# Kernel tuning notes

Measured on AMD Instinct MI355X. Metric: run time of the kernel, lower is better.

The kernel has to match this reference:

```python
import math
import jax, jax.numpy as jnp
import numpy as np

H = 8
DIM = 256
HD = DIM // H
SCALE = math.sqrt(HD)
EPS = 1e-16


def _segment_softmax(scores, dst, num_nodes):
    # scores: [E, H], dst: [E] -> softmax over edges sharing the same dst
    m = jax.ops.segment_max(scores, dst, num_segments=num_nodes)  # [N, H]
    m = jnp.where(jnp.isfinite(m), m, 0.0)  # empty segments -> -inf -> 0
    e = jnp.exp(scores - m[dst])
    s = jax.ops.segment_sum(e, dst, num_segments=num_nodes)  # [N, H]
    return e / (s[dst] + EPS)


def _graph_attention(x, edges, wq, bq, wk, bk, wv, bv, wo, bo):
    # x: [N, DIM]; edges: [2, E] (src, dst). Dropout is identity (eval mode).
    N = x.shape[0]
    Q = (x @ wq + bq).reshape(N, H, HD)
    K = (x @ wk + bk).reshape(N, H, HD)
    V = (x @ wv + bv).reshape(N, H, HD)
    src, dst = edges[0], edges[1]
    scores = jnp.einsum('ehd,ehd->eh', Q[dst], K[src]) / SCALE  # [E, H]
    attn = _segment_softmax(scores, dst, N)  # [E, H]
    msgs = V[src] * attn[:, :, None]  # [E, H, HD]
    out = jax.ops.segment_sum(msgs, dst, num_segments=N).reshape(N, DIM)
    return out @ wo + bo


def _linear_params(key, fan_in, fan_out):
    k1, k2 = jax.random.split(key)
    bound = 1.0 / math.sqrt(fan_in)
    w = jax.random.uniform(k1, (fan_in, fan_out), minval=-bound, maxval=bound, dtype=jnp.float32)
    b = jax.random.uniform(k2, (fan_out,), minval=-bound, maxval=bound, dtype=jnp.float32)
    return w, b


def setup_inputs() -> dict:
    key = jax.random.key(0)
    ks = jax.random.split(key, 12)
    n_slot, n_dom = 20000, 1000
    e_slot, e_dom = 320000, 16000
    inp = {
        'slot_x': jax.random.normal(ks[0], (n_slot, DIM), dtype=jnp.float32),
        'domain_x': jax.random.normal(ks[1], (n_dom, DIM), dtype=jnp.float32),
        'slot_edges': jax.random.randint(ks[2], (2, e_slot), 0, n_slot, dtype=jnp.int32),
        'domain_edges': jax.random.randint(ks[3], (2, e_dom), 0, n_dom, dtype=jnp.int32),
    }
    names = ['wq', 'wk', 'wv', 'wo']
    for i, nm in enumerate(names):
        w, b = _linear_params(ks[4 + i], DIM, DIM)
        inp[f'slot_{nm}'] = w
        inp[f'slot_{nm}_b'] = b
    for i, nm in enumerate(names):
        w, b = _linear_params(ks[8 + i], DIM, DIM)
        inp[f'dom_{nm}'] = w
        inp[f'dom_{nm}_b'] = b
    return inp


def reference(slot_x, domain_x, slot_edges, domain_edges,
              slot_wq, slot_wq_b, slot_wk, slot_wk_b, slot_wv, slot_wv_b, slot_wo, slot_wo_b,
              dom_wq, dom_wq_b, dom_wk, dom_wk_b, dom_wv, dom_wv_b, dom_wo, dom_wo_b):
    # slot branch: self-attention on slot graph + identity residual
    slot_out = _graph_attention(slot_x, slot_edges,
                                slot_wq, slot_wq_b, slot_wk, slot_wk_b,
                                slot_wv, slot_wv_b, slot_wo, slot_wo_b) + slot_x
    # domain branch
    dom_out = _graph_attention(domain_x, domain_edges,
                               dom_wq, dom_wq_b, dom_wk, dom_wk_b,
                               dom_wv, dom_wv_b, dom_wo, dom_wo_b) + domain_x
    return slot_out, dom_out
```

## Files before the change

### kernel.cpp

```cpp
#include <hip/hip_runtime.h>
#include <hip/hip_bf16.h>

#define DIM 256
#define INV_SCALE 0.17677669529663687f
#define SM_EPS 1e-16f
#define CAP 64
#define EPT 4

typedef unsigned short ushortT;
typedef unsigned int uintT;
typedef __attribute__((ext_vector_type(8))) __bf16 bf16x8;
typedef __attribute__((ext_vector_type(4))) float f32x4;

__device__ __forceinline__ float bf2f(ushortT u) {
    return __uint_as_float(((uintT)u) << 16);
}
__device__ __forceinline__ ushortT f2bf(float f) {
    uintT u = __float_as_uint(f);
    u += 0x7FFFu + ((u >> 16) & 1u);
    return (ushortT)(u >> 16);
}
template <int CTRL>
__device__ __forceinline__ float qperm_add(float p) {
    int v = __builtin_amdgcn_update_dpp(0, __float_as_int(p), CTRL, 0xF, 0xF, true);
    return p + __int_as_float(v);
}

struct WPack { const void* w[8]; const void* b[8]; };

__device__ __forceinline__ bool sniff_m16(const ushortT* __restrict__ x) {
    int lane = threadIdx.x & 63;
    ushortT u = x[lane * 2];
    int e = (u >> 7) & 0xFF;
    bool sane = ((u & 0x7FFFu) == 0) || (e >= 0x66 && e <= 0x90);
    unsigned long long m = __ballot(sane);
    return __popcll(m) >= 32;
}

__global__ __launch_bounds__(256) void megaA(
        const void* __restrict__ xs, const void* __restrict__ xd,
        const ushortT* __restrict__ sniff_src,
        ushortT* __restrict__ xb_s, ushortT* __restrict__ xb_d,
        WPack pk, ushortT* __restrict__ wT, float* __restrict__ biasF,
        int* __restrict__ flagWs,
        const int* __restrict__ src_s, const int* __restrict__ dst_s,
        const int* __restrict__ src_d, const int* __restrict__ dst_d,
        int* __restrict__ cnt_s, int* __restrict__ cnt_d,
        int* __restrict__ col_s, int* __restrict__ col_d,
        int Es_, int Ed_, int nSc,
        int n4s, int n4d, int nA0, int nA1)
{
    const int bid = blockIdx.x;
    const int t = threadIdx.x;

    if (bid < nSc) {
        const int base = bid * (256 * EPT) + t;
        #pragma unroll
        for (int u = 0; u < EPT; ++u) {
            const int idx = base + u * 256;
            if (idx < Es_) {
                const int dv = dst_s[idx];
                const int pos = atomicAdd(&cnt_s[dv], 1);
                if (pos < CAP) col_s[(dv << 6) + pos] = src_s[idx];
            } else {
                const int e = idx - Es_;
                if (e < Ed_) {
                    const int dv = dst_d[e];
                    const int pos = atomicAdd(&cnt_d[dv], 1);
                    if (pos < CAP) col_d[(dv << 6) + pos] = src_d[e];
                }
            }
        }
        return;
    }
    const bool m16 = sniff_m16(sniff_src);
    const int li2 = bid - nSc;

    if (li2 < nA0 + nA1) {
        const bool d = li2 >= nA0;
        const int li = d ? li2 - nA0 : li2;
        const int n4 = d ? n4d : n4s;
        const int i = li * 256 + t;
        if (i >= n4) return;
        const void* x = d ? xd : xs;
        ushortT* xb = d ? xb_d : xb_s;
        if (m16) {
            ((ushort4*)xb)[i] = ((const ushort4*)x)[i];
        } else {
            float4 v = ((const float4*)x)[i];
            ushort4 o2;
            o2.x = f2bf(v.x); o2.y = f2bf(v.y); o2.z = f2bf(v.z); o2.w = f2bf(v.w);
            ((ushort4*)xb)[i] = o2;
        }
    } else if (li2 < nA0 + nA1 + 128) {
        __shared__ float sh[64][65];
        const int r0 = li2 - (nA0 + nA1);
        const int which = r0 >> 4;
        const int tile = r0 & 15;
        const int tr = tile >> 2, tc = tile & 3;
        const void* w = pk.w[which];
        const int tx = t & 63, tg = t >> 6;
        #pragma unroll
        for (int i = 0; i < 16; ++i) {
            const int r = i * 4 + tg;
            const size_t si = (size_t)(tr * 64 + r) * 256 + tc * 64 + tx;
            sh[r][tx] = m16 ? bf2f(((const ushortT*)w)[si]) : ((const float*)w)[si];
        }
        __syncthreads();
        ushortT* o = wT + (size_t)which * 65536;
        #pragma unroll
        for (int i = 0; i < 16; ++i) {
            const int r = i * 4 + tg;
            o[(size_t)(tc * 64 + r) * 256 + tr * 64 + tx] = f2bf(sh[tx][r]);
        }
    } else if (li2 < nA0 + nA1 + 136) {
        const int which = li2 - (nA0 + nA1 + 128);
        const void* b = pk.b[which];
        float v = m16 ? bf2f(((const ushortT*)b)[t]) : ((const float*)b)[t];
        biasF[which * 256 + t] = v;
    } else {
        if (t == 0) *flagWs = m16 ? 1 : 0;
    }
}

__global__ __launch_bounds__(256, 2) void megaB(
        const ushortT* __restrict__ xb_s, const ushortT* __restrict__ xb_d,
        const ushortT* __restrict__ wT, const float* __restrict__ biasF,
        ushortT* __restrict__ q_s, ushortT* __restrict__ kv_s,
        ushortT* __restrict__ q_d, ushortT* __restrict__ kv_d,
        int Ms, int Md, int nbs_, int nbq_)
{
    const int bid = blockIdx.x;
    const int by  = bid / nbq_;
    const int bx0 = bid % nbq_;
    const bool dom = bx0 >= nbs_;
    const int bx = dom ? bx0 - nbs_ : bx0;
    const ushortT* A = dom ? xb_d : xb_s;
    const int M = dom ? Md : Ms;
    const int wbase = dom ? 4 : 0;
    ushortT* Q = dom ? q_d : q_s;
    ushortT* KV = dom ? kv_d : kv_s;

    __shared__ ushortT As[64 * 256];

    const int tid  = threadIdx.x;
    const int wid  = tid >> 6;
    const int lane = tid & 63;
    const int m    = lane & 15;
    const int q    = lane >> 4;
    const int row0 = bx * 64;
    const int col0 = by * 64;
    const int colw = col0 + wid * 16 + m;

    {
        const int r  = tid >> 2;
        const int qt = tid & 3;
        const size_t rowAddr = (size_t)min(row0 + r, M - 1) * DIM;
        const int xr = r & 7;
        #pragma unroll
        for (int j = 0; j < 8; ++j) {
            const int chunk = qt * 8 + j;
            uint4 v = *(const uint4*)(A + rowAddr + chunk * 8);
            *(uint4*)&As[r * 256 + ((chunk ^ xr) * 8)] = v;
        }
    }

    const ushortT* Bp = wT + (size_t)wbase * 65536 + (size_t)colw * DIM + q * 8;
    bf16x8 bl[8][3];
    #pragma unroll
    for (int kk = 0; kk < 8; ++kk)
        #pragma unroll
        for (int z = 0; z < 3; ++z)
            bl[kk][z] = *(const bf16x8*)(Bp + (size_t)z * 65536 + kk * 32);

    f32x4 acc[3][4];
    #pragma unroll
    for (int z = 0; z < 3; ++z)
        #pragma unroll
        for (int i = 0; i < 4; ++i)
            acc[z][i] = (f32x4){0.f, 0.f, 0.f, 0.f};

    const int xm = m & 7;

    __syncthreads();

    #pragma unroll
    for (int kk = 0; kk < 8; ++kk) {
        bf16x8 af[4];
        #pragma unroll
        for (int i = 0; i < 4; ++i)
            af[i] = *(const bf16x8*)&As[(i * 16 + m) * 256 + (((q + 4 * kk) ^ xm) * 8)];
        #pragma unroll
        for (int z = 0; z < 3; ++z)
            #pragma unroll
            for (int i = 0; i < 4; ++i)
                acc[z][i] = __builtin_amdgcn_mfma_f32_16x16x32_bf16(bl[kk][z], af[i], acc[z][i], 0, 0, 0);
    }

    const int colbase = col0 + wid * 16 + q * 4;
    #pragma unroll
    for (int z = 0; z < 3; ++z) {
        const float4 b4 = *(const float4*)&biasF[(wbase + z) * 256 + colbase];
        #pragma unroll
        for (int i = 0; i < 4; ++i) {
            const int row = row0 + i * 16 + m;
            if (row < M) {
                ushort4 o;
                o.x = f2bf(acc[z][i][0] + b4.x);
                o.y = f2bf(acc[z][i][1] + b4.y);
                o.z = f2bf(acc[z][i][2] + b4.z);
                o.w = f2bf(acc[z][i][3] + b4.w);
                ushortT* C = (z == 0)
                    ? (Q + (size_t)row * DIM + colbase)
                    : (KV + (size_t)row * 512 + (z - 1) * 256 + colbase);
                *(ushort4*)C = o;
            }
        }
    }
}

__global__ __launch_bounds__(256) void attn_kernel(
        const ushortT* __restrict__ Qs, const ushortT* __restrict__ KVs,
        const int* __restrict__ cnts, const int* __restrict__ css,
        ushortT* __restrict__ aggs,
        const ushortT* __restrict__ Qd_, const ushortT* __restrict__ KVd_,
        const int* __restrict__ cntd, const int* __restrict__ csd,
        ushortT* __restrict__ aggd,
        int Ns_, int Ntot)
{
    const int g = blockIdx.x * 4 + (threadIdx.x >> 6);
    if (g >= Ntot) return;
    const bool dom = g >= Ns_;
    const int d = dom ? g - Ns_ : g;
    const int t = threadIdx.x & 63;
    const ushortT* Qb = dom ? Qd_ : Qs;
    const ushortT* KVb = dom ? KVd_ : KVs;
    const int* cnt = dom ? cntd : cnts;
    const int* colsrc = dom ? csd : css;
    ushortT* aggb = dom ? aggd : aggs;

    const uintT t4 = (uintT)t * 4;
    const size_t cbase = (size_t)d * DIM + t4;
    uint2 qv = *(const uint2*)(Qb + cbase);
    const float q0 = bf2f((ushortT)(qv.x & 0xFFFF)), q1 = bf2f((ushortT)(qv.x >> 16));
    const float q2 = bf2f((ushortT)(qv.y & 0xFFFF)), q3 = bf2f((ushortT)(qv.y >> 16));

    float a0 = 0.f, a1 = 0.f, a2 = 0.f, a3 = 0.f, den = 0.f;

    auto PROC = [&](uint2 kvc, uint2 vvc) {
        float k0 = bf2f((ushortT)(kvc.x & 0xFFFF)), k1 = bf2f((ushortT)(kvc.x >> 16));
        float k2 = bf2f((ushortT)(kvc.y & 0xFFFF)), k3 = bf2f((ushortT)(kvc.y >> 16));
        float p = q0 * k0 + q1 * k1 + q2 * k2 + q3 * k3;
        p = qperm_add<0xB1>(p);
        p = qperm_add<0x4E>(p);
        p += __shfl_xor(p, 4, 8);
        const float w = __expf(fminf(p * INV_SCALE, 60.0f));
        den += w;
        a0 += w * bf2f((ushortT)(vvc.x & 0xFFFF));
        a1 += w * bf2f((ushortT)(vvc.x >> 16));
        a2 += w * bf2f((ushortT)(vvc.y & 0xFFFF));
        a3 += w * bf2f((ushortT)(vvc.y >> 16));
    };

    int deg = cnt[d];
    if (deg > CAP) deg = CAP;
    const int* cl = colsrc + ((size_t)d << 6);
    int i = 0;
    for (; i + 8 <= deg; i += 8) {
        const int4 c0 = *(const int4*)(cl + i);
        const int4 c1 = *(const int4*)(cl + i + 4);
        const uintT o0 = ((uintT)c0.x << 9) + t4;
        const uintT o1 = ((uintT)c0.y << 9) + t4;
        const uintT o2 = ((uintT)c0.z << 9) + t4;
        const uintT o3 = ((uintT)c0.w << 9) + t4;
        const uintT o4 = ((uintT)c1.x << 9) + t4;
        const uintT o5 = ((uintT)c1.y << 9) + t4;
        const uintT o6 = ((uintT)c1.z << 9) + t4;
        const uintT o7 = ((uintT)c1.w << 9) + t4;
        uint2 k0v = *(const uint2*)(KVb + o0), v0v = *(const uint2*)(KVb + o0 + 256);
        uint2 k1v = *(const uint2*)(KVb + o1), v1v = *(const uint2*)(KVb + o1 + 256);
        uint2 k2v = *(const uint2*)(KVb + o2), v2v = *(const uint2*)(KVb + o2 + 256);
        uint2 k3v = *(const uint2*)(KVb + o3), v3v = *(const uint2*)(KVb + o3 + 256);
        uint2 k4v = *(const uint2*)(KVb + o4), v4v = *(const uint2*)(KVb + o4 + 256);
        uint2 k5v = *(const uint2*)(KVb + o5), v5v = *(const uint2*)(KVb + o5 + 256);
        uint2 k6v = *(const uint2*)(KVb + o6), v6v = *(const uint2*)(KVb + o6 + 256);
        uint2 k7v = *(const uint2*)(KVb + o7), v7v = *(const uint2*)(KVb + o7 + 256);
        PROC(k0v, v0v); PROC(k1v, v1v); PROC(k2v, v2v); PROC(k3v, v3v);
        PROC(k4v, v4v); PROC(k5v, v5v); PROC(k6v, v6v); PROC(k7v, v7v);
    }
    for (; i + 4 <= deg; i += 4) {
        const int4 c0 = *(const int4*)(cl + i);
        const uintT o0 = ((uintT)c0.x << 9) + t4;
        const uintT o1 = ((uintT)c0.y << 9) + t4;
        const uintT o2 = ((uintT)c0.z << 9) + t4;
        const uintT o3 = ((uintT)c0.w << 9) + t4;
        uint2 k0v = *(const uint2*)(KVb + o0), v0v = *(const uint2*)(KVb + o0 + 256);
        uint2 k1v = *(const uint2*)(KVb + o1), v1v = *(const uint2*)(KVb + o1 + 256);
        uint2 k2v = *(const uint2*)(KVb + o2), v2v = *(const uint2*)(KVb + o2 + 256);
        uint2 k3v = *(const uint2*)(KVb + o3), v3v = *(const uint2*)(KVb + o3 + 256);
        PROC(k0v, v0v); PROC(k1v, v1v); PROC(k2v, v2v); PROC(k3v, v3v);
    }
    for (; i < deg; ++i) {
        const uintT sb = ((uintT)cl[i] << 9) + t4;
        uint2 kv = *(const uint2*)(KVb + sb);
        uint2 vv = *(const uint2*)(KVb + sb + 256);
        PROC(kv, vv);
    }

    const float r = 1.0f / (den + SM_EPS);
    ushort4 o;
    o.x = f2bf(a0 * r); o.y = f2bf(a1 * r); o.z = f2bf(a2 * r); o.w = f2bf(a3 * r);
    *(ushort4*)(aggb + cbase) = o;
}

__global__ __launch_bounds__(256, 2) void gemm_out(
        const ushortT* __restrict__ As_, const ushortT* __restrict__ Ad_,
        const ushortT* __restrict__ wT, const float* __restrict__ biasF,
        const void* __restrict__ xs, const void* __restrict__ xd,
        void* __restrict__ dout, int Ms, int Md, int nbs,
        const int* __restrict__ flag)
{
    const bool dom = (int)blockIdx.x >= nbs;
    const int bx = dom ? blockIdx.x - nbs : blockIdx.x;
    const ushortT* A = dom ? Ad_ : As_;
    const int M = dom ? Md : Ms;
    const int widx = 3 + (dom ? 4 : 0);
    const ushortT* BT = wT + (size_t)widx * 65536;
    const float* bias = biasF + widx * 256;
    const void* res = dom ? xd : xs;
    const size_t outOff = dom ? (size_t)Ms * DIM : 0;

    __shared__ ushortT As2[64 * 256];

    const int tid  = threadIdx.x;
    const int wid  = tid >> 6;
    const int lane = tid & 63;
    const int m    = lane & 15;
    const int q    = lane >> 4;
    const int row0 = bx * 64;
    const int col0 = blockIdx.y * 64;
    const int colw = col0 + wid * 16 + m;

    {
        const int r  = tid >> 2;
        const int qt = tid & 3;
        const size_t rowAddr = (size_t)min(row0 + r, M - 1) * DIM;
        const int xr = r & 7;
        #pragma unroll
        for (int j = 0; j < 8; ++j) {
            const int chunk = qt * 8 + j;
            uint4 v = *(const uint4*)(A + rowAddr + chunk * 8);
            *(uint4*)&As2[r * 256 + ((chunk ^ xr) * 8)] = v;
        }
    }

    const ushortT* Bp = BT + (size_t)colw * DIM + q * 8;
    bf16x8 bl[8];
    #pragma unroll
    for (int kk = 0; kk < 8; ++kk)
        bl[kk] = *(const bf16x8*)(Bp + kk * 32);

    f32x4 acc[4];
    #pragma unroll
    for (int i = 0; i < 4; ++i) acc[i] = (f32x4){0.f, 0.f, 0.f, 0.f};

    const int xm = m & 7;

    __syncthreads();

    #pragma unroll
    for (int kk = 0; kk < 8; ++kk) {
        bf16x8 af[4];
        #pragma unroll
        for (int i = 0; i < 4; ++i)
            af[i] = *(const bf16x8*)&As2[(i * 16 + m) * 256 + (((q + 4 * kk) ^ xm) * 8)];
        #pragma unroll
        for (int i = 0; i < 4; ++i)
            acc[i] = __builtin_amdgcn_mfma_f32_16x16x32_bf16(bl[kk], af[i], acc[i], 0, 0, 0);
    }

    const bool m16 = (*flag != 0);
    const int colbase = col0 + wid * 16 + q * 4;
    const float4 b4 = *(const float4*)&bias[colbase];
    #pragma unroll
    for (int i = 0; i < 4; ++i) {
        const int row = row0 + i * 16 + m;
        if (row < M) {
            const size_t ridx = (size_t)row * DIM + colbase;
            float v0 = acc[i][0] + b4.x, v1 = acc[i][1] + b4.y;
            float v2 = acc[i][2] + b4.z, v3 = acc[i][3] + b4.w;
            if (m16) {
                ushort4 rv = *(const ushort4*)((const ushortT*)res + ridx);
                v0 += bf2f(rv.x); v1 += bf2f(rv.y); v2 += bf2f(rv.z); v3 += bf2f(rv.w);
                ushort4 o;
                o.x = f2bf(v0); o.y = f2bf(v1); o.z = f2bf(v2); o.w = f2bf(v3);
                *(ushort4*)((ushortT*)dout + outOff + ridx) = o;
            } else {
                float4 rv = *(const float4*)((const float*)res + ridx);
                float4 o;
                o.x = v0 + rv.x; o.y = v1 + rv.y; o.z = v2 + rv.z; o.w = v3 + rv.w;
                *(float4*)((float*)dout + outOff + ridx) = o;
            }
        }
    }
}

extern "C" void kernel_launch(void* const* d_in, const int* in_sizes, int n_in,
                              void* d_out, int out_size, void* d_ws, size_t ws_size,
                              hipStream_t stream)
{
    const void* slot_x = d_in[0];
    const void* dom_x  = d_in[1];
    const int* slot_edges = (const int*)d_in[2];
    const int* dom_edges  = (const int*)d_in[3];
    const int Ns = in_sizes[0] / DIM;
    const int Nd = in_sizes[1] / DIM;
    const int Es = in_sizes[2] / 2;
    const int Ed = in_sizes[3] / 2;

    WPack pk;
    for (int i = 0; i < 8; ++i) { pk.w[i] = d_in[4 + 2 * i]; pk.b[i] = d_in[5 + 2 * i]; }

    char* p = (char*)d_ws;
    size_t o = 0;
    auto take = [&](size_t b) { void* r = p + o; o = (o + b + 255) & ~(size_t)255; return r; };
    const size_t ndS = (size_t)Ns * DIM;
    const size_t ndD = (size_t)Nd * DIM;
    ushortT* xb_s  = (ushortT*)take(ndS * 2);
    ushortT* q_s   = (ushortT*)take(ndS * 2);
    ushortT* kv_s  = (ushortT*)take(2 * ndS * 2);
    ushortT* agg_s = (ushortT*)take(ndS * 2);
    ushortT* xb_d  = (ushortT*)take(ndD * 2);
    ushortT* q_d   = (ushortT*)take(ndD * 2);
    ushortT* kv_d  = (ushortT*)take(2 * ndD * 2);
    ushortT* agg_d = (ushortT*)take(ndD * 2);
    ushortT* wT    = (ushortT*)take(8 * 65536 * 2);
    float*   biasF = (float*)take(8 * 256 * 4);
    int* cnt_s = (int*)take((size_t)(Ns + Nd) * 4);
    int* cnt_d = cnt_s + Ns;
    int* col_s = (int*)take((size_t)Ns * CAP * 4);
    int* col_d = (int*)take((size_t)Nd * CAP * 4);
    int* flagWs = (int*)take(256);

    const int* src_s = slot_edges;
    const int* dst_s = slot_edges + Es;
    const int* src_d = dom_edges;
    const int* dst_d = dom_edges + Ed;

    const int n4s = Ns * DIM / 4, n4d = Nd * DIM / 4;
    const int nbs = (Ns + 63) / 64;
    const int nbd = (Nd + 63) / 64;
    const int nbq = nbs + nbd;

    (void)hipMemsetAsync(cnt_s, 0, (size_t)(Ns + Nd) * 4, stream);

    const int Etot = Es + Ed;
    const int nSc = (Etot + 256 * EPT - 1) / (256 * EPT);
    const int nA0 = (n4s + 255) / 256;
    const int nA1 = (n4d + 255) / 256;
    hipLaunchKernelGGL(megaA, dim3(nSc + nA0 + nA1 + 136 + 1), dim3(256), 0, stream,
                       slot_x, dom_x, (const ushortT*)slot_x, xb_s, xb_d,
                       pk, wT, biasF, flagWs,
                       src_s, dst_s, src_d, dst_d,
                       cnt_s, cnt_d, col_s, col_d,
                       Es, Ed, nSc, n4s, n4d, nA0, nA1);

    hipLaunchKernelGGL(megaB, dim3(nbq * 4), dim3(256), 0, stream,
                       xb_s, xb_d, wT, biasF, q_s, kv_s, q_d, kv_d,
                       Ns, Nd, nbs, nbq);

    const int Ntot = Ns + Nd;
    hipLaunchKernelGGL(attn_kernel, dim3((Ntot + 3) / 4), dim3(256), 0, stream,
                       q_s, kv_s, cnt_s, col_s, agg_s,
                       q_d, kv_d, cnt_d, col_d, agg_d,
                       Ns, Ntot);

    hipLaunchKernelGGL(gemm_out, dim3(nbq, DIM / 64), dim3(256), 0, stream,
                       agg_s, agg_d, wT, biasF, slot_x, dom_x, d_out,
                       Ns, Nd, nbs, flagWs);
}
```

Before: 225.7 us.

## Fuse pipeline into one cooperative persistent kernel with grid syncs

Replaces the memset plus four kernel launches with a single cooperative persistent kernel. Phases are separated by grid.sync and the kernel loops over virtual blocks: weight/bias prep and counter zeroing, then edge scatter with the QKV GEMM, then attention, then the output GEMM. The x-to-bf16 conversion is folded into the QKV GEMM's shared-memory load, which removes the xb buffers and the flag readback. The goal is to cut launch overhead and the intermediate pass over x. In exchange it adds grid-wide barriers, a persistent grid capped by occupancy, and a fallback path of separate launches.

```diff
diff --git a/kernel.cpp b/kernel.cpp
--- a/kernel.cpp
+++ b/kernel.cpp
@@ -1,5 +1,8 @@
 #include <hip/hip_runtime.h>
 #include <hip/hip_bf16.h>
+#include <hip/hip_cooperative_groups.h>
+
+namespace cg = cooperative_groups;
 
 #define DIM 256
 #define INV_SCALE 0.17677669529663687f
@@ -37,68 +40,30 @@
     return __popcll(m) >= 32;
 }
 
-__global__ __launch_bounds__(256) void megaA(
-        const void* __restrict__ xs, const void* __restrict__ xd,
-        const ushortT* __restrict__ sniff_src,
-        ushortT* __restrict__ xb_s, ushortT* __restrict__ xb_d,
-        WPack pk, ushortT* __restrict__ wT, float* __restrict__ biasF,
-        int* __restrict__ flagWs,
-        const int* __restrict__ src_s, const int* __restrict__ dst_s,
-        const int* __restrict__ src_d, const int* __restrict__ dst_d,
-        int* __restrict__ cnt_s, int* __restrict__ cnt_d,
-        int* __restrict__ col_s, int* __restrict__ col_d,
-        int Es_, int Ed_, int nSc,
-        int n4s, int n4d, int nA0, int nA1)
-{
-    const int bid = blockIdx.x;
+struct KP {
+    const void* xs; const void* xd;
+    const ushortT* sniff;
+    const int* src_s; const int* dst_s;
+    const int* src_d; const int* dst_d;
+    WPack pk;
+    ushortT* wT; float* biasF;
+    ushortT* q_s; ushortT* kv_s; ushortT* q_d; ushortT* kv_d;
+    ushortT* agg_s; ushortT* agg_d;
+    int* cnt_s; int* cnt_d; int* col_s; int* col_d;
+    void* dout;
+    int Ns, Nd, Es, Ed, nbs, nbq, nSc, nZ, nAttn, nGemm;
+};
+
+
+__device__ __forceinline__ void body_prep(int vb, bool m16, const KP& P, void* smem)
+{
     const int t = threadIdx.x;
-
-    if (bid < nSc) {
-        const int base = bid * (256 * EPT) + t;
-        #pragma unroll
-        for (int u = 0; u < EPT; ++u) {
-            const int idx = base + u * 256;
-            if (idx < Es_) {
-                const int dv = dst_s[idx];
-                const int pos = atomicAdd(&cnt_s[dv], 1);
-                if (pos < CAP) col_s[(dv << 6) + pos] = src_s[idx];
-            } else {
-                const int e = idx - Es_;
-                if (e < Ed_) {
-                    const int dv = dst_d[e];
-                    const int pos = atomicAdd(&cnt_d[dv], 1);
-                    if (pos < CAP) col_d[(dv << 6) + pos] = src_d[e];
-                }
-            }
-        }
-        return;
-    }
-    const bool m16 = sniff_m16(sniff_src);
-    const int li2 = bid - nSc;
-
-    if (li2 < nA0 + nA1) {
-        const bool d = li2 >= nA0;
-        const int li = d ? li2 - nA0 : li2;
-        const int n4 = d ? n4d : n4s;
-        const int i = li * 256 + t;
-        if (i >= n4) return;
-        const void* x = d ? xd : xs;
-        ushortT* xb = d ? xb_d : xb_s;
-        if (m16) {
-            ((ushort4*)xb)[i] = ((const ushort4*)x)[i];
-        } else {
-            float4 v = ((const float4*)x)[i];
-            ushort4 o2;
-            o2.x = f2bf(v.x); o2.y = f2bf(v.y); o2.z = f2bf(v.z); o2.w = f2bf(v.w);
-            ((ushort4*)xb)[i] = o2;
-        }
-    } else if (li2 < nA0 + nA1 + 128) {
-        __shared__ float sh[64][65];
-        const int r0 = li2 - (nA0 + nA1);
-        const int which = r0 >> 4;
-        const int tile = r0 & 15;
+    if (vb < 128) {
+        float (*sh)[65] = (float(*)[65])smem;
+        const int which = vb >> 4;
+        const int tile = vb & 15;
         const int tr = tile >> 2, tc = tile & 3;
-        const void* w = pk.w[which];
+        const void* w = P.pk.w[which];
         const int tx = t & 63, tg = t >> 6;
         #pragma unroll
         for (int i = 0; i < 16; ++i) {
@@ -107,65 +72,95 @@
             sh[r][tx] = m16 ? bf2f(((const ushortT*)w)[si]) : ((const float*)w)[si];
         }
         __syncthreads();
-        ushortT* o = wT + (size_t)which * 65536;
+        ushortT* o = P.wT + (size_t)which * 65536;
         #pragma unroll
         for (int i = 0; i < 16; ++i) {
             const int r = i * 4 + tg;
             o[(size_t)(tc * 64 + r) * 256 + tr * 64 + tx] = f2bf(sh[tx][r]);
         }
-    } else if (li2 < nA0 + nA1 + 136) {
-        const int which = li2 - (nA0 + nA1 + 128);
-        const void* b = pk.b[which];
+        __syncthreads();
+    } else {
+        const int which = vb - 128;
+        const void* b = P.pk.b[which];
         float v = m16 ? bf2f(((const ushortT*)b)[t]) : ((const float*)b)[t];
-        biasF[which * 256 + t] = v;
-    } else {
-        if (t == 0) *flagWs = m16 ? 1 : 0;
-    }
-}
-
-__global__ __launch_bounds__(256, 2) void megaB(
-        const ushortT* __restrict__ xb_s, const ushortT* __restrict__ xb_d,
-        const ushortT* __restrict__ wT, const float* __restrict__ biasF,
-        ushortT* __restrict__ q_s, ushortT* __restrict__ kv_s,
-        ushortT* __restrict__ q_d, ushortT* __restrict__ kv_d,
-        int Ms, int Md, int nbs_, int nbq_)
-{
-    const int bid = blockIdx.x;
-    const int by  = bid / nbq_;
-    const int bx0 = bid % nbq_;
-    const bool dom = bx0 >= nbs_;
-    const int bx = dom ? bx0 - nbs_ : bx0;
-    const ushortT* A = dom ? xb_d : xb_s;
-    const int M = dom ? Md : Ms;
+        P.biasF[which * 256 + t] = v;
+    }
+}
+
+__device__ __forceinline__ void body_scatter(int vb, const KP& P)
+{
+    const int base = vb * (256 * EPT) + threadIdx.x;
+    #pragma unroll
+    for (int u = 0; u < EPT; ++u) {
+        const int idx = base + u * 256;
+        if (idx < P.Es) {
+            const int dv = P.dst_s[idx];
+            const int pos = atomicAdd(&P.cnt_s[dv], 1);
+            if (pos < CAP) P.col_s[(dv << 6) + pos] = P.src_s[idx];
+        } else {
+            const int e = idx - P.Es;
+            if (e < P.Ed) {
+                const int dv = P.dst_d[e];
+                const int pos = atomicAdd(&P.cnt_d[dv], 1);
+                if (pos < CAP) P.col_d[(dv << 6) + pos] = P.src_d[e];
+            }
+        }
+    }
+}
+
+__device__ __forceinline__ void body_qkvgemm(int gv, bool m16, const KP& P, ushortT* As)
+{
+    const int tid = threadIdx.x;
+    const int by  = gv / P.nbq;
+    const int bx0 = gv % P.nbq;
+    const bool dom = bx0 >= P.nbs;
+    const int bx = dom ? bx0 - P.nbs : bx0;
+    const void* X = dom ? P.xd : P.xs;
+    const int M = dom ? P.Nd : P.Ns;
     const int wbase = dom ? 4 : 0;
-    ushortT* Q = dom ? q_d : q_s;
-    ushortT* KV = dom ? kv_d : kv_s;
-
-    __shared__ ushortT As[64 * 256];
-
-    const int tid  = threadIdx.x;
-    const int wid  = tid >> 6;
+    ushortT* Q = dom ? P.q_d : P.q_s;
+    ushortT* KV = dom ? P.kv_d : P.kv_s;
+
+    const int wid = tid >> 6;
     const int lane = tid & 63;
-    const int m    = lane & 15;
-    const int q    = lane >> 4;
+    const int m = lane & 15;
+    const int q = lane >> 4;
     const int row0 = bx * 64;
     const int col0 = by * 64;
     const int colw = col0 + wid * 16 + m;
 
+    __syncthreads();
     {
         const int r  = tid >> 2;
         const int qt = tid & 3;
-        const size_t rowAddr = (size_t)min(row0 + r, M - 1) * DIM;
         const int xr = r & 7;
-        #pragma unroll
-        for (int j = 0; j < 8; ++j) {
-            const int chunk = qt * 8 + j;
-            uint4 v = *(const uint4*)(A + rowAddr + chunk * 8);
-            *(uint4*)&As[r * 256 + ((chunk ^ xr) * 8)] = v;
-        }
-    }
-
-    const ushortT* Bp = wT + (size_t)wbase * 65536 + (size_t)colw * DIM + q * 8;
+        const int row = min(row0 + r, M - 1);
+        if (m16) {
+            const ushortT* src = (const ushortT*)X + (size_t)row * DIM;
+            #pragma unroll
+            for (int j = 0; j < 8; ++j) {
+                const int chunk = qt * 8 + j;
+                uint4 v = *(const uint4*)(src + chunk * 8);
+                *(uint4*)&As[r * 256 + ((chunk ^ xr) * 8)] = v;
+            }
+        } else {
+            const float* src = (const float*)X + (size_t)row * DIM;
+            #pragma unroll
+            for (int j = 0; j < 8; ++j) {
+                const int chunk = qt * 8 + j;
+                float4 f0 = *(const float4*)(src + chunk * 8);
+                float4 f1 = *(const float4*)(src + chunk * 8 + 4);
+                ushort4 a, b;
+                a.x = f2bf(f0.x); a.y = f2bf(f0.y); a.z = f2bf(f0.z); a.w = f2bf(f0.w);
+                b.x = f2bf(f1.x); b.y = f2bf(f1.y); b.z = f2bf(f1.z); b.w = f2bf(f1.w);
+                ushortT* d = &As[r * 256 + ((chunk ^ xr) * 8)];
+                *(ushort4*)d = a;
+                *(ushort4*)(d + 4) = b;
+            }
+        }
+    }
+
+    const ushortT* Bp = P.wT + (size_t)wbase * 65536 + (size_t)colw * DIM + q * 8;
     bf16x8 bl[8][3];
     #pragma unroll
     for (int kk = 0; kk < 8; ++kk)
@@ -181,7 +176,6 @@
             acc[z][i] = (f32x4){0.f, 0.f, 0.f, 0.f};
 
     const int xm = m & 7;
-
     __syncthreads();
 
     #pragma unroll
@@ -200,7 +194,7 @@
     const int colbase = col0 + wid * 16 + q * 4;
     #pragma unroll
     for (int z = 0; z < 3; ++z) {
-        const float4 b4 = *(const float4*)&biasF[(wbase + z) * 256 + colbase];
+        const float4 b4 = *(const float4*)&P.biasF[(wbase + z) * 256 + colbase];
         #pragma unroll
         for (int i = 0; i < 4; ++i) {
             const int row = row0 + i * 16 + m;
@@ -219,25 +213,19 @@
     }
 }
 
-__global__ __launch_bounds__(256) void attn_kernel(
-        const ushortT* __restrict__ Qs, const ushortT* __restrict__ KVs,
-        const int* __restrict__ cnts, const int* __restrict__ css,
-        ushortT* __restrict__ aggs,
-        const ushortT* __restrict__ Qd_, const ushortT* __restrict__ KVd_,
-        const int* __restrict__ cntd, const int* __restrict__ csd,
-        ushortT* __restrict__ aggd,
-        int Ns_, int Ntot)
-{
-    const int g = blockIdx.x * 4 + (threadIdx.x >> 6);
+__device__ __forceinline__ void body_attn(int vb, const KP& P)
+{
+    const int Ntot = P.Ns + P.Nd;
+    const int g = vb * 4 + (threadIdx.x >> 6);
     if (g >= Ntot) return;
-    const bool dom = g >= Ns_;
-    const int d = dom ? g - Ns_ : g;
+    const bool dom = g >= P.Ns;
+    const int d = dom ? g - P.Ns : g;
     const int t = threadIdx.x & 63;
-    const ushortT* Qb = dom ? Qd_ : Qs;
-    const ushortT* KVb = dom ? KVd_ : KVs;
-    const int* cnt = dom ? cntd : cnts;
-    const int* colsrc = dom ? csd : css;
-    ushortT* aggb = dom ? aggd : aggs;
+    const ushortT* Qb = dom ? P.q_d : P.q_s;
+    const ushortT* KVb = dom ? P.kv_d : P.kv_s;
+    const int* cnt = dom ? P.cnt_d : P.cnt_s;
+    const int* colsrc = dom ? P.col_d : P.col_s;
+    ushortT* aggb = dom ? P.agg_d : P.agg_s;
 
     const uintT t4 = (uintT)t * 4;
     const size_t cbase = (size_t)d * DIM + t4;
@@ -313,34 +301,30 @@
     *(ushort4*)(aggb + cbase) = o;
 }
 
-__global__ __launch_bounds__(256, 2) void gemm_out(
-        const ushortT* __restrict__ As_, const ushortT* __restrict__ Ad_,
-        const ushortT* __restrict__ wT, const float* __restrict__ biasF,
-        const void* __restrict__ xs, const void* __restrict__ xd,
-        void* __restrict__ dout, int Ms, int Md, int nbs,
-        const int* __restrict__ flag)
-{
-    const bool dom = (int)blockIdx.x >= nbs;
-    const int bx = dom ? blockIdx.x - nbs : blockIdx.x;
-    const ushortT* A = dom ? Ad_ : As_;
-    const int M = dom ? Md : Ms;
+__device__ __forceinline__ void body_outgemm(int gv, bool m16, const KP& P, ushortT* As2)
+{
+    const int tid = threadIdx.x;
+    const int by  = gv / P.nbq;
+    const int bx0 = gv % P.nbq;
+    const bool dom = bx0 >= P.nbs;
+    const int bx = dom ? bx0 - P.nbs : bx0;
+    const ushortT* A = dom ? P.agg_d : P.agg_s;
+    const int M = dom ? P.Nd : P.Ns;
     const int widx = 3 + (dom ? 4 : 0);
-    const ushortT* BT = wT + (size_t)widx * 65536;
-    const float* bias = biasF + widx * 256;
-    const void* res = dom ? xd : xs;
-    const size_t outOff = dom ? (size_t)Ms * DIM : 0;
-
-    __shared__ ushortT As2[64 * 256];
-
-    const int tid  = threadIdx.x;
+    const ushortT* BT = P.wT + (size_t)widx * 65536;
+    const float* bias = P.biasF + widx * 256;
+    const void* res = dom ? P.xd : P.xs;
+    const size_t outOff = dom ? (size_t)P.Ns * DIM : 0;
+
     const int wid  = tid >> 6;
     const int lane = tid & 63;
     const int m    = lane & 15;
     const int q    = lane >> 4;
     const int row0 = bx * 64;
-    const int col0 = blockIdx.y * 64;
+    const int col0 = by * 64;
     const int colw = col0 + wid * 16 + m;
 
+    __syncthreads();
     {
         const int r  = tid >> 2;
         const int qt = tid & 3;
@@ -365,7 +349,6 @@
     for (int i = 0; i < 4; ++i) acc[i] = (f32x4){0.f, 0.f, 0.f, 0.f};
 
     const int xm = m & 7;
-
     __syncthreads();
 
     #pragma unroll
@@ -379,7 +362,6 @@
             acc[i] = __builtin_amdgcn_mfma_f32_16x16x32_bf16(bl[kk], af[i], acc[i], 0, 0, 0);
     }
 
-    const bool m16 = (*flag != 0);
     const int colbase = col0 + wid * 16 + q * 4;
     const float4 b4 = *(const float4*)&bias[colbase];
     #pragma unroll
@@ -394,15 +376,75 @@
                 v0 += bf2f(rv.x); v1 += bf2f(rv.y); v2 += bf2f(rv.z); v3 += bf2f(rv.w);
                 ushort4 o;
                 o.x = f2bf(v0); o.y = f2bf(v1); o.z = f2bf(v2); o.w = f2bf(v3);
-                *(ushort4*)((ushortT*)dout + outOff + ridx) = o;
+                *(ushort4*)((ushortT*)P.dout + outOff + ridx) = o;
             } else {
                 float4 rv = *(const float4*)((const float*)res + ridx);
                 float4 o;
                 o.x = v0 + rv.x; o.y = v1 + rv.y; o.z = v2 + rv.z; o.w = v3 + rv.w;
-                *(float4*)((float*)dout + outOff + ridx) = o;
+                *(float4*)((float*)P.dout + outOff + ridx) = o;
             }
         }
     }
+}
+
+__global__ __launch_bounds__(256, 2) void mega(KP P)
+{
+    __shared__ char smemRaw[64 * 256 * 2];
+    cg::grid_group grid = cg::this_grid();
+    const bool m16 = sniff_m16(P.sniff);
+    const int Ntot = P.Ns + P.Nd;
+
+    const int nP0 = 136 + P.nZ;
+    for (int vb = blockIdx.x; vb < nP0; vb += gridDim.x) {
+        if (vb < 136) {
+            body_prep(vb, m16, P, smemRaw);
+        } else {
+            const int idx = (vb - 136) * 256 + threadIdx.x;
+            if (idx < Ntot) P.cnt_s[idx] = 0;
+        }
+    }
+    grid.sync();
+
+    for (int vb = blockIdx.x; vb < P.nSc + P.nGemm; vb += gridDim.x) {
+        if (vb < P.nSc) body_scatter(vb, P);
+        else            body_qkvgemm(vb - P.nSc, m16, P, (ushortT*)smemRaw);
+    }
+    grid.sync();
+
+    for (int vb = blockIdx.x; vb < P.nAttn; vb += gridDim.x)
+        body_attn(vb, P);
+    grid.sync();
+
+    for (int vb = blockIdx.x; vb < P.nGemm; vb += gridDim.x)
+        body_outgemm(vb, m16, P, (ushortT*)smemRaw);
+}
+
+__global__ __launch_bounds__(256) void k_prep(KP P)
+{
+    const bool m16 = sniff_m16(P.sniff);
+    __shared__ char smem[64 * 65 * 4];
+    body_prep(blockIdx.x, m16, P, smem);
+}
+
+__global__ __launch_bounds__(256, 2) void k_scatgemm(KP P)
+{
+    __shared__ ushortT As[64 * 256];
+    const int bid = blockIdx.x;
+    if (bid < P.nSc) { body_scatter(bid, P); return; }
+    const bool m16 = sniff_m16(P.sniff);
+    body_qkvgemm(bid - P.nSc, m16, P, As);
+}
+
+__global__ __launch_bounds__(256) void k_attn(KP P)
+{
+    body_attn(blockIdx.x, P);
+}
+
+__global__ __launch_bounds__(256, 2) void k_outgemm(KP P)
+{
+    __shared__ ushortT As2[64 * 256];
+    const bool m16 = sniff_m16(P.sniff);
+    body_outgemm(blockIdx.x, m16, P, As2);
 }
 
 extern "C" void kernel_launch(void* const* d_in, const int* in_sizes, int n_in,
@@ -426,11 +468,9 @@
     auto take = [&](size_t b) { void* r = p + o; o = (o + b + 255) & ~(size_t)255; return r; };
     const size_t ndS = (size_t)Ns * DIM;
     const size_t ndD = (size_t)Nd * DIM;
-    ushortT* xb_s  = (ushortT*)take(ndS * 2);
     ushortT* q_s   = (ushortT*)take(ndS * 2);
     ushortT* kv_s  = (ushortT*)take(2 * ndS * 2);
     ushortT* agg_s = (ushortT*)take(ndS * 2);
-    ushortT* xb_d  = (ushortT*)take(ndD * 2);
     ushortT* q_d   = (ushortT*)take(ndD * 2);
     ushortT* kv_d  = (ushortT*)take(2 * ndD * 2);
     ushortT* agg_d = (ushortT*)take(ndD * 2);
@@ -440,42 +480,50 @@
     int* cnt_d = cnt_s + Ns;
     int* col_s = (int*)take((size_t)Ns * CAP * 4);
     int* col_d = (int*)take((size_t)Nd * CAP * 4);
-    int* flagWs = (int*)take(256);
-
-    const int* src_s = slot_edges;
-    const int* dst_s = slot_edges + Es;
-    const int* src_d = dom_edges;
-    const int* dst_d = dom_edges + Ed;
-
-    const int n4s = Ns * DIM / 4, n4d = Nd * DIM / 4;
+
     const int nbs = (Ns + 63) / 64;
     const int nbd = (Nd + 63) / 64;
     const int nbq = nbs + nbd;
 
-    (void)hipMemsetAsync(cnt_s, 0, (size_t)(Ns + Nd) * 4, stream);
-
-    const int Etot = Es + Ed;
-    const int nSc = (Etot + 256 * EPT - 1) / (256 * EPT);
-    const int nA0 = (n4s + 255) / 256;
-    const int nA1 = (n4d + 255) / 256;
-    hipLaunchKernelGGL(megaA, dim3(nSc + nA0 + nA1 + 136 + 1), dim3(256), 0, stream,
-                       slot_x, dom_x, (const ushortT*)slot_x, xb_s, xb_d,
-                       pk, wT, biasF, flagWs,
-                       src_s, dst_s, src_d, dst_d,
-                       cnt_s, cnt_d, col_s, col_d,
-                       Es, Ed, nSc, n4s, n4d, nA0, nA1);
-
-    hipLaunchKernelGGL(megaB, dim3(nbq * 4), dim3(256), 0, stream,
-                       xb_s, xb_d, wT, biasF, q_s, kv_s, q_d, kv_d,
-                       Ns, Nd, nbs, nbq);
-
-    const int Ntot = Ns + Nd;
-    hipLaunchKernelGGL(attn_kernel, dim3((Ntot + 3) / 4), dim3(256), 0, stream,
-                       q_s, kv_s, cnt_s, col_s, agg_s,
-                       q_d, kv_d, cnt_d, col_d, agg_d,
-                       Ns, Ntot);
-
-    hipLaunchKernelGGL(gemm_out, dim3(nbq, DIM / 64), dim3(256), 0, stream,
-                       agg_s, agg_d, wT, biasF, slot_x, dom_x, d_out,
-                       Ns, Nd, nbs, flagWs);
-}
+    KP hp;
+    hp.xs = slot_x; hp.xd = dom_x;
+    hp.sniff = (const ushortT*)slot_x;
+    hp.src_s = slot_edges; hp.dst_s = slot_edges + Es;
+    hp.src_d = dom_edges;  hp.dst_d = dom_edges + Ed;
+    hp.pk = pk;
+    hp.wT = wT; hp.biasF = biasF;
+    hp.q_s = q_s; hp.kv_s = kv_s; hp.q_d = q_d; hp.kv_d = kv_d;
+    hp.agg_s = agg_s; hp.agg_d = agg_d;
+    hp.cnt_s = cnt_s; hp.cnt_d = cnt_d; hp.col_s = col_s; hp.col_d = col_d;
+    hp.dout = d_out;
+    hp.Ns = Ns; hp.Nd = Nd; hp.Es = Es; hp.Ed = Ed;
+    hp.nbs = nbs; hp.nbq = nbq;
+    hp.nSc = (Es + Ed + 256 * EPT - 1) / (256 * EPT);
+    hp.nZ  = (Ns + Nd + 255) / 256;
+    hp.nAttn = (Ns + Nd + 3) / 4;
+    hp.nGemm = 4 * nbq;
+
+    hipError_t cerr = hipErrorUnknown;
+    int maxB = 0;
+    if (hipOccupancyMaxActiveBlocksPerMultiprocessor(&maxB, (const void*)mega,
+                                                     256, 0) == hipSuccess &&
+        maxB > 0) {
+        int numCU = 0;
+        if (hipDeviceGetAttribute(&numCU, hipDeviceAttributeMultiprocessorCount, 0)
+                != hipSuccess || numCU <= 0)
+            numCU = 256;
+        int nblk = maxB * numCU;
+        void* args[] = { &hp };
+        cerr = hipLaunchCooperativeKernel((const void*)mega, dim3(nblk),
+                                          dim3(256), args, 0, stream);
+    }
+
+    if (cerr != hipSuccess) {
+        (void)hipMemsetAsync(cnt_s, 0, (size_t)(Ns + Nd) * 4, stream);
+        void* args[] = { &hp };
+        (void)hipLaunchKernel((const void*)k_prep, dim3(136), dim3(256), args, 0, stream);
+        (void)hipLaunchKernel((const void*)k_scatgemm, dim3(hp.nSc + hp.nGemm), dim3(256), args, 0, stream);
+        (void)hipLaunchKernel((const void*)k_attn, dim3(hp.nAttn), dim3(256), args, 0, stream);
+        (void)hipLaunchKernel((const void*)k_outgemm, dim3(hp.nGemm), dim3(256), args, 0, stream);
+    }
+}
```

After: 395.4 us. +75.2%, slower.
